# Kernel tuning notes

Hardware: AMD Instinct MI355X
Metric: run time of the kernel (lower is better)

## Reference

```python
import jax, jax.numpy as jnp
import numpy as np

B, T = 256, 1024
IN, OUT = 1, 1
H0, H1 = 256, 256


def _lstm_cell(x_t, h, c, W_ih, W_hh, b_ih, b_hh):
    # gates: [B, 4H] in torch LSTMCell order i, f, g, o
    g = x_t @ W_ih.T + b_ih + h @ W_hh.T + b_hh
    i, f, gg, o = jnp.split(g, 4, axis=-1)
    c_new = jax.nn.sigmoid(f) * c + jax.nn.sigmoid(i) * jnp.tanh(gg)
    h_new = jax.nn.sigmoid(o) * jnp.tanh(c_new)
    return h_new, c_new


def setup_inputs() -> dict:
    key = jax.random.key(0)
    ks = jax.random.split(key, 12)
    s = 0.1
    return {
        "x": jax.random.normal(ks[0], (B, T), dtype=jnp.float32),
        "W_ih0": jax.random.normal(ks[1], (4 * H0, IN), dtype=jnp.float32) * s,
        "W_hh0": jax.random.normal(ks[2], (4 * H0, H0), dtype=jnp.float32) * s,
        "b_ih0": jax.random.normal(ks[3], (4 * H0,), dtype=jnp.float32) * s,
        "b_hh0": jax.random.normal(ks[4], (4 * H0,), dtype=jnp.float32) * s,
        "W_ih1": jax.random.normal(ks[5], (4 * H1, H0), dtype=jnp.float32) * s,
        "W_hh1": jax.random.normal(ks[6], (4 * H1, H1), dtype=jnp.float32) * s,
        "b_ih1": jax.random.normal(ks[7], (4 * H1,), dtype=jnp.float32) * s,
        "b_hh1": jax.random.normal(ks[8], (4 * H1,), dtype=jnp.float32) * s,
        "W_lin": jax.random.normal(ks[9], (OUT, H1), dtype=jnp.float32) * s,
        "b_lin": jax.random.normal(ks[10], (OUT,), dtype=jnp.float32) * s,
        "future": 0,
    }


def reference(x, W_ih0, W_hh0, b_ih0, b_hh0, W_ih1, W_hh1, b_ih1, b_hh1,
              W_lin, b_lin, future):
    b = x.shape[0]
    h0 = jnp.zeros((b, H0), x.dtype)
    c0 = jnp.zeros((b, H0), x.dtype)
    h1 = jnp.zeros((b, H1), x.dtype)
    c1 = jnp.zeros((b, H1), x.dtype)

    def step(carry, x_t):
        ht, ct, gt, bt = carry
        ht, ct = _lstm_cell(x_t, ht, ct, W_ih0, W_hh0, b_ih0, b_hh0)
        gt, bt = _lstm_cell(ht, gt, bt, W_ih1, W_hh1, b_ih1, b_hh1)
        out = gt @ W_lin.T + b_lin  # [B, OUT]
        return (ht, ct, gt, bt), out

    xs = x.T[:, :, None]  # [T, B, 1]
    carry, outs = jax.lax.scan(step, (h0, c0, h1, c1), xs)

    if future > 0:
        def fstep(carry, _):
            state, out = carry
            state, out = step(state, out)
            return (state, out), out
        (_, _), fouts = jax.lax.scan(fstep, (carry, outs[-1]), None, length=future)
        outs = jnp.concatenate([outs, fouts], axis=0)

    # stack dim 1 then squeeze(2): [B, T+future]
    return jnp.transpose(outs, (1, 0, 2)).squeeze(2)
```

## Files before the change

kernel.cpp:

```cpp
#include <hip/hip_runtime.h>
#include <hip/hip_bf16.h>
#include <stdint.h>


#define TT 1024
#define NC 16

typedef __attribute__((ext_vector_type(8))) short  bfrag;
typedef __attribute__((ext_vector_type(4))) float  ffrag;

__device__ __forceinline__ float sigf(float v){ return 1.f/(1.f+__expf(-v)); }
__device__ __forceinline__ float tanhfast(float v){
    v = fminf(fmaxf(v,-15.f),15.f);
    float e = __expf(2.f*v);
    return (e-1.f)/(e+1.f);
}
__device__ __forceinline__ void st32(uint32_t* p, uint32_t v){
    __hip_atomic_store(p, v, __ATOMIC_RELAXED, __HIP_MEMORY_SCOPE_AGENT);
}
__device__ __forceinline__ void st64(unsigned long long* p, unsigned long long v){
    __hip_atomic_store(p, v, __ATOMIC_RELAXED, __HIP_MEMORY_SCOPE_AGENT);
}
__device__ __forceinline__ void stf(float* p, float v){
    __hip_atomic_store(p, v, __ATOMIC_RELAXED, __HIP_MEMORY_SCOPE_AGENT);
}
__device__ __forceinline__ void drain_vmem(){
    __asm__ volatile("s_waitcnt vmcnt(0)" ::: "memory");
}
__device__ __forceinline__ float2 ldf2_coh(const float* p1, const float* p2){
    float a, b;
    __asm__ volatile(
        "global_load_dword %0, %2, off sc0 sc1\n\t"
        "global_load_dword %1, %3, off sc0 sc1\n\t"
        "s_waitcnt vmcnt(0)"
        : "=&v"(a), "=&v"(b) : "v"(p1), "v"(p2) : "memory");
    return make_float2(a, b);
}
__device__ __forceinline__ void prefetch4(const int* fa, const int* fb,
                                          const int* fc, const int* fd,
                                          int& va, int& vb, int& vc, int& vd){
    __asm__ volatile(
        "global_load_dword %0, %4, off sc0 sc1\n\t"
        "global_load_dword %1, %5, off sc0 sc1\n\t"
        "global_load_dword %2, %6, off sc0 sc1\n\t"
        "global_load_dword %3, %7, off sc0 sc1"
        : "=&v"(va), "=&v"(vb), "=&v"(vc), "=&v"(vd)
        : "v"(fa), "v"(fb), "v"(fc), "v"(fd) : "memory");
}
__device__ __forceinline__ void wave_poll_pf(const int* fa, const int* fb,
                                             const int* fc, const int* fd,
                                             int tgtA, int tgtB,
                                             bool skA, bool skB, bool skC, bool skD,
                                             int& va, int& vb, int& vc, int& vd){
    __asm__ volatile("s_waitcnt vmcnt(0)"
                     : "+v"(va), "+v"(vb), "+v"(vc), "+v"(vd) :: "memory");
    __builtin_amdgcn_sched_barrier(0);
    if ((skA || va >= tgtA) && (skB || vb >= tgtA) &&
        (skC || vc >= tgtB) && (skD || vd >= tgtB)) return;
    for (;;) {
        __asm__ volatile(
            "global_load_dword %0, %4, off sc0 sc1\n\t"
            "global_load_dword %1, %5, off sc0 sc1\n\t"
            "global_load_dword %2, %6, off sc0 sc1\n\t"
            "global_load_dword %3, %7, off sc0 sc1\n\t"
            "s_waitcnt vmcnt(0)"
            : "=&v"(va), "=&v"(vb), "=&v"(vc), "=&v"(vd)
            : "v"(fa), "v"(fb), "v"(fc), "v"(fd) : "memory");
        if (va >= tgtA && vb >= tgtA && vc >= tgtB && vd >= tgtB) return;
        __builtin_amdgcn_s_sleep(1);
    }
}
__device__ __forceinline__ void stage_tile(uint32_t* ldsbase, const uint32_t* hblocks,
                                           int kt, int lane){
    const uint32_t* g = hblocks + (kt << 8) + ((lane & 15) << 4) + ((lane >> 4) << 2);
    uint32_t* l = ldsbase + (kt << 8);
    __builtin_amdgcn_global_load_lds(
        (const __attribute__((address_space(1))) uint32_t*)(uintptr_t)g,
        (__attribute__((address_space(3))) uint32_t*)(uint32_t)(uintptr_t)l,
        16, 0, 0x11);
}
__device__ __forceinline__ void xpose4(ffrag& a, int lane){
    float x0 = (lane&1) ? a[0] : a[1];
    float y0 = __shfl_xor(x0, 1);
    a[0] = (lane&1) ? y0 : a[0];  a[1] = (lane&1) ? a[1] : y0;
    float x1 = (lane&1) ? a[2] : a[3];
    float y1 = __shfl_xor(x1, 1);
    a[2] = (lane&1) ? y1 : a[2];  a[3] = (lane&1) ? a[3] : y1;
    float x2 = (lane&2) ? a[0] : a[2];
    float y2 = __shfl_xor(x2, 2);
    a[0] = (lane&2) ? y2 : a[0];  a[2] = (lane&2) ? a[2] : y2;
    float x3 = (lane&2) ? a[1] : a[3];
    float y3 = __shfl_xor(x3, 2);
    a[1] = (lane&2) ? y3 : a[1];  a[3] = (lane&2) ? a[3] : y3;
}

__global__ void __launch_bounds__(256, 1)
lstm_kernel(const float* __restrict__ x,
            const float* __restrict__ Wih0, const float* __restrict__ Whh0,
            const float* __restrict__ bih0, const float* __restrict__ bhh0,
            const float* __restrict__ Wih1, const float* __restrict__ Whh1,
            const float* __restrict__ bih1, const float* __restrict__ bhh1,
            const float* __restrict__ Wlin, const float* __restrict__ blin,
            float* __restrict__ out, char* __restrict__ ws)
{
    const int tid = threadIdx.x;
    const int wg  = blockIdx.x;
    const int c   = wg >> 4;
    const int j   = wg & 15;
    const bool isL0 = (j < 8);
    const int  u0   = (isL0 ? j : (j - 8)) * 32;

    int* flagbase = (int*)(ws + c * 4096);
    uint32_t* h0w = (uint32_t*)(ws + 65536);
    uint32_t* h1w = h0w + 4 * NC * 8 * 256;
    float*    op  = (float*)(h1w + 4 * NC * 8 * 256);

    __shared__ __attribute__((aligned(16))) char S[147456];
    __hip_bfloat16* Wt  = (__hip_bfloat16*)S;
    __hip_bfloat16* Wt2 = (__hip_bfloat16*)(S + 65536);
    float*          xs  = (float*)(S + 65536);
    uint32_t*       hs0 = (uint32_t*)(S + 131072);
    uint32_t*       hs1 = (uint32_t*)(S + 139264);

    const int lane = tid & 63, wave = tid >> 6;
    const int q_l  = (lane >> 2) & 3;
    const int g_l  = lane & 3;
    const int rg   = lane >> 4;
    const int row  = rg * 4 + g_l;
    const int u_e  = wave * 8 + q_l * 2;

    {
        const float* Wsrc = isL0 ? Whh0 : Wih1;
        for (int i = tid; i < 128 * 256; i += 256) {
            int n = i >> 8, k = i & 255;
            int ntile = n >> 4, cc = n & 15, q = cc >> 2, g = cc & 3;
            int unit = 8 * (ntile >> 1) + 2 * q + (ntile & 1);
            int r = g * 256 + u0 + unit;
            int ln = (n & 15) | (((k >> 3) & 3) << 4);
            int toff = (ntile * 8 + (k >> 5)) * 1024 + ln * 16 + (k & 7) * 2;
            *(__hip_bfloat16*)((char*)Wt + toff) = __float2bfloat16(Wsrc[r * 256 + k]);
            if (!isL0)
                *(__hip_bfloat16*)((char*)Wt2 + toff) = __float2bfloat16(Whh1[r * 256 + k]);
        }
        if (isL0) {
            for (int i = tid; i < 16 * 1024; i += 256)
                xs[i] = x[(c * 16 + (i & 15)) * TT + (i >> 4)];
        }
        uint32_t* z = isL0 ? (h0w + ((3 * NC + c) * 8 + j) * 256)
                           : (h1w + ((3 * NC + c) * 8 + (j - 8)) * 256);
        st32(z + tid, 0u);
    }
    float be0,be1,be2,be3, bo0,bo1,bo2,bo3;
    float we0=0,we1=0,we2=0,we3=0, wo0=0,wo1=0,wo2=0,wo3=0;
    float wle=0, wlo=0;
    {
        const float* bi = isL0 ? bih0 : bih1;
        const float* bh = isL0 ? bhh0 : bhh1;
        int r0 = u0 + u_e;
        be0 = bi[r0] + bh[r0];               bo0 = bi[r0+1] + bh[r0+1];
        be1 = bi[256+r0] + bh[256+r0];       bo1 = bi[256+r0+1] + bh[256+r0+1];
        be2 = bi[512+r0] + bh[512+r0];       bo2 = bi[512+r0+1] + bh[512+r0+1];
        be3 = bi[768+r0] + bh[768+r0];       bo3 = bi[768+r0+1] + bh[768+r0+1];
        if (isL0) {
            we0 = Wih0[r0];     wo0 = Wih0[r0+1];
            we1 = Wih0[256+r0]; wo1 = Wih0[256+r0+1];
            we2 = Wih0[512+r0]; wo2 = Wih0[512+r0+1];
            we3 = Wih0[768+r0]; wo3 = Wih0[768+r0+1];
        } else {
            wle = Wlin[u0 + u_e]; wlo = Wlin[u0 + u_e + 1];
        }
    }
    const float blin_r = blin[0];
    drain_vmem();
    __syncthreads();
    if (tid == 0) st32((uint32_t*)(flagbase + j * 32), 0u);

    const int* fL0a = flagbase + (wave)      * 32;
    const int* fL0b = flagbase + (wave + 4)  * 32;
    const int* fL1a = flagbase + (8 + wave)  * 32;
    const int* fL1b = flagbase + (12 + wave) * 32;
    int* myflag = (int*)(flagbase + j * 32);
    const bool skA = isL0 && (j == wave);
    const bool skB = isL0 && (j == wave + 4);
    const bool skC = (!isL0) && (j - 8 == wave);
    const bool skD = (!isL0) && (j - 8 == wave + 4);
    int va = -1000, vb = -1000, vc = -1000, vd = -1000;

    const char* wb0 = (const char*)Wt + (wave * 2) * 8192 + lane * 16;
    const char* wb1 = wb0 + 8192;
    const char* wc0 = (const char*)Wt2 + (wave * 2) * 8192 + lane * 16;
    const char* wc1 = wc0 + 8192;

    float c0a = 0.f, c0b = 0.f;

    if (isL0) {
        for (int t = 0; t < TT; ++t) {
            wave_poll_pf(fL0a, fL0b, fL1a, fL1b, t, t - 2,
                         skA, skB, false, false, va, vb, vc, vd);
            const uint32_t* src = h0w + (((t + 3) & 3) * NC + c) * 8 * 256;
            stage_tile(hs0, src, wave, lane);
            stage_tile(hs0, src, wave + 4, lane);
            __syncthreads();

            ffrag a0 = {0.f,0.f,0.f,0.f}, a1 = {0.f,0.f,0.f,0.f};
            #pragma unroll
            for (int kt = 0; kt < 8; ++kt) {
                bfrag av = *(const bfrag*)((const char*)hs0 + kt * 1024 + lane * 16);
                bfrag b0 = *(const bfrag*)(wb0 + kt * 1024);
                bfrag b1 = *(const bfrag*)(wb1 + kt * 1024);
                a0 = __builtin_amdgcn_mfma_f32_16x16x32_bf16(av, b0, a0, 0, 0, 0);
                a1 = __builtin_amdgcn_mfma_f32_16x16x32_bf16(av, b1, a1, 0, 0, 0);
            }
            xpose4(a0, lane);
            xpose4(a1, lane);

            float xv = xs[t * 16 + row];
            float iv = a0[0] + fmaf(xv, we0, be0);
            float fv = a0[1] + fmaf(xv, we1, be1);
            float gv = a0[2] + fmaf(xv, we2, be2);
            float ov = a0[3] + fmaf(xv, we3, be3);
            c0a = sigf(fv) * c0a + sigf(iv) * tanhfast(gv);
            float hn0 = sigf(ov) * tanhfast(c0a);
            iv = a1[0] + fmaf(xv, wo0, bo0);
            fv = a1[1] + fmaf(xv, wo1, bo1);
            gv = a1[2] + fmaf(xv, wo2, bo2);
            ov = a1[3] + fmaf(xv, wo3, bo3);
            c0b = sigf(fv) * c0b + sigf(iv) * tanhfast(gv);
            float hn1 = sigf(ov) * tanhfast(c0b);

            __hip_bfloat16 hb0 = __float2bfloat16(hn0), hb1 = __float2bfloat16(hn1);
            uint32_t pk = ((uint32_t)(*(uint16_t*)&hb1) << 16) | (uint32_t)(*(uint16_t*)&hb0);
            uint32_t nb = __shfl_down(pk, 4);
            if ((q_l & 1) == 0) {
                unsigned long long v = (unsigned long long)pk |
                                       ((unsigned long long)nb << 32);
                st64((unsigned long long*)
                     (h0w + (((t & 3) * NC + c) * 8 + j) * 256 + row * 16 + wave * 4 + q_l), v);
            }
            prefetch4(fL0a, fL0b, fL1a, fL1b, va, vb, vc, vd);
            drain_vmem();
            __syncthreads();
            if (tid == 0) st32((uint32_t*)myflag, (uint32_t)(t + 1));

            if (t >= 3 && j == ((t - 3) & 7)) {
                int col = t - 3, slot = col & 3;
                const float* o1 = op + (((slot * NC + c) * 32) + (tid & 15)) * 16 + (tid >> 4);
                float2 vv = ldf2_coh(o1, o1 + 256);
                float v = vv.x + vv.y;
                v += __shfl_down(v, 8, 16);
                v += __shfl_down(v, 4, 16);
                v += __shfl_down(v, 2, 16);
                v += __shfl_down(v, 1, 16);
                if ((tid & 15) == 0) out[(c * 16 + (tid >> 4)) * TT + col] = v + blin_r;
            }
        }
    } else {
        for (int t = 0; t < TT; ++t) {
            wave_poll_pf(fL0a, fL0b, fL1a, fL1b, t + 1, t,
                         false, false, skC, skD, va, vb, vc, vd);
            const uint32_t* s0 = h0w + ((t & 3) * NC + c) * 8 * 256;
            const uint32_t* s1 = h1w + (((t + 3) & 3) * NC + c) * 8 * 256;
            stage_tile(hs0, s0, wave, lane);
            stage_tile(hs0, s0, wave + 4, lane);
            stage_tile(hs1, s1, wave, lane);
            stage_tile(hs1, s1, wave + 4, lane);
            __syncthreads();

            ffrag a0 = {0.f,0.f,0.f,0.f}, a1 = {0.f,0.f,0.f,0.f};
            #pragma unroll
            for (int kt = 0; kt < 8; ++kt) {
                bfrag av = *(const bfrag*)((const char*)hs0 + kt * 1024 + lane * 16);
                bfrag b0 = *(const bfrag*)(wb0 + kt * 1024);
                bfrag b1 = *(const bfrag*)(wb1 + kt * 1024);
                a0 = __builtin_amdgcn_mfma_f32_16x16x32_bf16(av, b0, a0, 0, 0, 0);
                a1 = __builtin_amdgcn_mfma_f32_16x16x32_bf16(av, b1, a1, 0, 0, 0);
            }
            #pragma unroll
            for (int kt = 0; kt < 8; ++kt) {
                bfrag av = *(const bfrag*)((const char*)hs1 + kt * 1024 + lane * 16);
                bfrag b0 = *(const bfrag*)(wc0 + kt * 1024);
                bfrag b1 = *(const bfrag*)(wc1 + kt * 1024);
                a0 = __builtin_amdgcn_mfma_f32_16x16x32_bf16(av, b0, a0, 0, 0, 0);
                a1 = __builtin_amdgcn_mfma_f32_16x16x32_bf16(av, b1, a1, 0, 0, 0);
            }
            xpose4(a0, lane);
            xpose4(a1, lane);

            float iv = a0[0] + be0, fv = a0[1] + be1;
            float gv = a0[2] + be2, ov = a0[3] + be3;
            c0a = sigf(fv) * c0a + sigf(iv) * tanhfast(gv);
            float hn0 = sigf(ov) * tanhfast(c0a);
            iv = a1[0] + bo0; fv = a1[1] + bo1;
            gv = a1[2] + bo2; ov = a1[3] + bo3;
            c0b = sigf(fv) * c0b + sigf(iv) * tanhfast(gv);
            float hn1 = sigf(ov) * tanhfast(c0b);

            __hip_bfloat16 hb0 = __float2bfloat16(hn0), hb1 = __float2bfloat16(hn1);
            uint32_t pk = ((uint32_t)(*(uint16_t*)&hb1) << 16) | (uint32_t)(*(uint16_t*)&hb0);
            uint32_t nb = __shfl_down(pk, 4);

            float pv = hn0 * wle + hn1 * wlo;
            pv += __shfl_xor(pv, 4);
            pv += __shfl_xor(pv, 8);

            if ((q_l & 1) == 0) {
                unsigned long long v = (unsigned long long)pk |
                                       ((unsigned long long)nb << 32);
                st64((unsigned long long*)
                     (h1w + (((t & 3) * NC + c) * 8 + (j - 8)) * 256 + row * 16 + wave * 4 + q_l), v);
            }
            if ((lane & 12) == 0)
                stf(op + ((((t & 3) * NC + c) * 32) + (j - 8) * 4 + wave) * 16 + row, pv);
            prefetch4(fL0a, fL0b, fL1a, fL1b, va, vb, vc, vd);
            drain_vmem();
            __syncthreads();
            if (tid == 0) st32((uint32_t*)myflag, (uint32_t)(t + 1));
        }
    }

    drain_vmem();

    if (isL0 && j >= 5) {
        wave_poll_pf(fL0a, fL0b, fL1a, fL1b, 0, TT,
                     true, true, false, false, va, vb, vc, vd);
        __syncthreads();
        int col = TT - 8 + j, slot = col & 3;
        const float* o1 = op + (((slot * NC + c) * 32) + (tid & 15)) * 16 + (tid >> 4);
        float2 vv = ldf2_coh(o1, o1 + 256);
        float v = vv.x + vv.y;
        v += __shfl_down(v, 8, 16);
        v += __shfl_down(v, 4, 16);
        v += __shfl_down(v, 2, 16);
        v += __shfl_down(v, 1, 16);
        if ((tid & 15) == 0) out[(c * 16 + (tid >> 4)) * TT + col] = v + blin_r;
    }
}

extern "C" void kernel_launch(void* const* d_in, const int* in_sizes, int n_in,
                              void* d_out, int out_size, void* d_ws, size_t ws_size,
                              hipStream_t stream)
{
    const float* x    = (const float*)d_in[0];
    const float* Wih0 = (const float*)d_in[1];
    const float* Whh0 = (const float*)d_in[2];
    const float* bih0 = (const float*)d_in[3];
    const float* bhh0 = (const float*)d_in[4];
    const float* Wih1 = (const float*)d_in[5];
    const float* Whh1 = (const float*)d_in[6];
    const float* bih1 = (const float*)d_in[7];
    const float* bhh1 = (const float*)d_in[8];
    const float* Wlin = (const float*)d_in[9];
    const float* blin = (const float*)d_in[10];
    float* out = (float*)d_out;
    char* ws   = (char*)d_ws;

    lstm_kernel<<<dim3(256), dim3(256), 0, stream>>>(
        x, Wih0, Whh0, bih0, bhh0, Wih1, Whh1, bih1, bhh1, Wlin, blin, out, ws);
}
```

Baseline: 3.284 ms.

## Process two batch chunks per workgroup and widen layer pipeline skew

Each workgroup now handles two 16-row batch chunks (A and B) instead of one, halving the grid to 128 workgroups and the number of groups that synchronize through global flags. Flags become 64-bit paired lines polled with dwordx2 loads and a wave-wide all-vote, with a bail-out counter. The layer-1 schedule now lags layer 0 by two steps, the output buffer ring grows to 8 slots, and the final linear reduction is deferred and batched for both chunks. This amortizes per-step sync latency over twice the MFMA work but doubles serial work per step per workgroup, and the bail-out could silently break correctness if polling stalls.

```diff
diff --git a/kernel.cpp b/kernel.cpp
--- a/kernel.cpp
+++ b/kernel.cpp
@@ -8,6 +8,7 @@
 
 typedef __attribute__((ext_vector_type(8))) short  bfrag;
 typedef __attribute__((ext_vector_type(4))) float  ffrag;
+typedef __attribute__((ext_vector_type(2))) int    i2v;
 
 __device__ __forceinline__ float sigf(float v){ return 1.f/(1.f+__expf(-v)); }
 __device__ __forceinline__ float tanhfast(float v){
@@ -26,49 +27,6 @@
 }
 __device__ __forceinline__ void drain_vmem(){
     __asm__ volatile("s_waitcnt vmcnt(0)" ::: "memory");
-}
-__device__ __forceinline__ float2 ldf2_coh(const float* p1, const float* p2){
-    float a, b;
-    __asm__ volatile(
-        "global_load_dword %0, %2, off sc0 sc1\n\t"
-        "global_load_dword %1, %3, off sc0 sc1\n\t"
-        "s_waitcnt vmcnt(0)"
-        : "=&v"(a), "=&v"(b) : "v"(p1), "v"(p2) : "memory");
-    return make_float2(a, b);
-}
-__device__ __forceinline__ void prefetch4(const int* fa, const int* fb,
-                                          const int* fc, const int* fd,
-                                          int& va, int& vb, int& vc, int& vd){
-    __asm__ volatile(
-        "global_load_dword %0, %4, off sc0 sc1\n\t"
-        "global_load_dword %1, %5, off sc0 sc1\n\t"
-        "global_load_dword %2, %6, off sc0 sc1\n\t"
-        "global_load_dword %3, %7, off sc0 sc1"
-        : "=&v"(va), "=&v"(vb), "=&v"(vc), "=&v"(vd)
-        : "v"(fa), "v"(fb), "v"(fc), "v"(fd) : "memory");
-}
-__device__ __forceinline__ void wave_poll_pf(const int* fa, const int* fb,
-                                             const int* fc, const int* fd,
-                                             int tgtA, int tgtB,
-                                             bool skA, bool skB, bool skC, bool skD,
-                                             int& va, int& vb, int& vc, int& vd){
-    __asm__ volatile("s_waitcnt vmcnt(0)"
-                     : "+v"(va), "+v"(vb), "+v"(vc), "+v"(vd) :: "memory");
-    __builtin_amdgcn_sched_barrier(0);
-    if ((skA || va >= tgtA) && (skB || vb >= tgtA) &&
-        (skC || vc >= tgtB) && (skD || vd >= tgtB)) return;
-    for (;;) {
-        __asm__ volatile(
-            "global_load_dword %0, %4, off sc0 sc1\n\t"
-            "global_load_dword %1, %5, off sc0 sc1\n\t"
-            "global_load_dword %2, %6, off sc0 sc1\n\t"
-            "global_load_dword %3, %7, off sc0 sc1\n\t"
-            "s_waitcnt vmcnt(0)"
-            : "=&v"(va), "=&v"(vb), "=&v"(vc), "=&v"(vd)
-            : "v"(fa), "v"(fb), "v"(fc), "v"(fd) : "memory");
-        if (va >= tgtA && vb >= tgtA && vc >= tgtB && vd >= tgtB) return;
-        __builtin_amdgcn_s_sleep(1);
-    }
 }
 __device__ __forceinline__ void stage_tile(uint32_t* ldsbase, const uint32_t* hblocks,
                                            int kt, int lane){
@@ -93,6 +51,30 @@
     float y3 = __shfl_xor(x3, 2);
     a[1] = (lane&2) ? y3 : a[1];  a[3] = (lane&2) ? a[3] : y3;
 }
+__device__ __forceinline__ void reduce2(const float* op, int cA, int cB, int col,
+                                        int tid, float blin_r, float* __restrict__ out){
+    int slot = col & 7;
+    const float* oA = op + ((slot * NC + cA) * 32 + (tid & 15)) * 16 + (tid >> 4);
+    const float* oB = op + ((slot * NC + cB) * 32 + (tid & 15)) * 16 + (tid >> 4);
+    float ra, rb, rc, rd;
+    __asm__ volatile(
+        "global_load_dword %0, %4, off sc0 sc1\n\t"
+        "global_load_dword %1, %5, off sc0 sc1\n\t"
+        "global_load_dword %2, %6, off sc0 sc1\n\t"
+        "global_load_dword %3, %7, off sc0 sc1\n\t"
+        "s_waitcnt vmcnt(0)"
+        : "=&v"(ra), "=&v"(rb), "=&v"(rc), "=&v"(rd)
+        : "v"(oA), "v"(oA + 256), "v"(oB), "v"(oB + 256) : "memory");
+    float vA = ra + rb, vB = rc + rd;
+    vA += __shfl_down(vA, 8, 16); vA += __shfl_down(vA, 4, 16);
+    vA += __shfl_down(vA, 2, 16); vA += __shfl_down(vA, 1, 16);
+    vB += __shfl_down(vB, 8, 16); vB += __shfl_down(vB, 4, 16);
+    vB += __shfl_down(vB, 2, 16); vB += __shfl_down(vB, 1, 16);
+    if ((tid & 15) == 0) {
+        out[(cA * 16 + (tid >> 4)) * TT + col] = vA + blin_r;
+        out[(cB * 16 + (tid >> 4)) * TT + col] = vB + blin_r;
+    }
+}
 
 __global__ void __launch_bounds__(256, 1)
 lstm_kernel(const float* __restrict__ x,
@@ -105,22 +87,23 @@
 {
     const int tid = threadIdx.x;
     const int wg  = blockIdx.x;
-    const int c   = wg >> 4;
+    const int g   = wg >> 4;
     const int j   = wg & 15;
     const bool isL0 = (j < 8);
     const int  u0   = (isL0 ? j : (j - 8)) * 32;
-
-    int* flagbase = (int*)(ws + c * 4096);
+    const int  cA = g * 2, cB = g * 2 + 1;
+
+    char* flg = ws + (size_t)g * 4096;
     uint32_t* h0w = (uint32_t*)(ws + 65536);
     uint32_t* h1w = h0w + 4 * NC * 8 * 256;
     float*    op  = (float*)(h1w + 4 * NC * 8 * 256);
 
-    __shared__ __attribute__((aligned(16))) char S[147456];
+    __shared__ __attribute__((aligned(16))) char S[155648];
     __hip_bfloat16* Wt  = (__hip_bfloat16*)S;
     __hip_bfloat16* Wt2 = (__hip_bfloat16*)(S + 65536);
-    float*          xs  = (float*)(S + 65536);
-    uint32_t*       hs0 = (uint32_t*)(S + 131072);
-    uint32_t*       hs1 = (uint32_t*)(S + 139264);
+    char* tA0 = S + 131072;
+    char* tA1 = S + 139264;
+    char* tB0 = S + 147456;
 
     const int lane = tid & 63, wave = tid >> 6;
     const int q_l  = (lane >> 2) & 3;
@@ -133,22 +116,21 @@
         const float* Wsrc = isL0 ? Whh0 : Wih1;
         for (int i = tid; i < 128 * 256; i += 256) {
             int n = i >> 8, k = i & 255;
-            int ntile = n >> 4, cc = n & 15, q = cc >> 2, g = cc & 3;
+            int ntile = n >> 4, cc = n & 15, q = cc >> 2, gg = cc & 3;
             int unit = 8 * (ntile >> 1) + 2 * q + (ntile & 1);
-            int r = g * 256 + u0 + unit;
+            int r = gg * 256 + u0 + unit;
             int ln = (n & 15) | (((k >> 3) & 3) << 4);
             int toff = (ntile * 8 + (k >> 5)) * 1024 + ln * 16 + (k & 7) * 2;
             *(__hip_bfloat16*)((char*)Wt + toff) = __float2bfloat16(Wsrc[r * 256 + k]);
             if (!isL0)
                 *(__hip_bfloat16*)((char*)Wt2 + toff) = __float2bfloat16(Whh1[r * 256 + k]);
         }
-        if (isL0) {
-            for (int i = tid; i < 16 * 1024; i += 256)
-                xs[i] = x[(c * 16 + (i & 15)) * TT + (i >> 4)];
-        }
-        uint32_t* z = isL0 ? (h0w + ((3 * NC + c) * 8 + j) * 256)
-                           : (h1w + ((3 * NC + c) * 8 + (j - 8)) * 256);
-        st32(z + tid, 0u);
+        uint32_t* zA = isL0 ? (h0w + ((3 * NC + cA) * 8 + j) * 256)
+                            : (h1w + ((3 * NC + cA) * 8 + (j - 8)) * 256);
+        uint32_t* zB = isL0 ? (h0w + ((3 * NC + cB) * 8 + j) * 256)
+                            : (h1w + ((3 * NC + cB) * 8 + (j - 8)) * 256);
+        st32(zA + tid, 0u);
+        st32(zB + tid, 0u);
     }
     float be0,be1,be2,be3, bo0,bo1,bo2,bo3;
     float we0=0,we1=0,we2=0,we3=0, wo0=0,wo1=0,wo2=0,wo3=0;
@@ -173,166 +155,261 @@
     const float blin_r = blin[0];
     drain_vmem();
     __syncthreads();
-    if (tid == 0) st32((uint32_t*)(flagbase + j * 32), 0u);
-
-    const int* fL0a = flagbase + (wave)      * 32;
-    const int* fL0b = flagbase + (wave + 4)  * 32;
-    const int* fL1a = flagbase + (8 + wave)  * 32;
-    const int* fL1b = flagbase + (12 + wave) * 32;
-    int* myflag = (int*)(flagbase + j * 32);
-    const bool skA = isL0 && (j == wave);
-    const bool skB = isL0 && (j == wave + 4);
-    const bool skC = (!isL0) && (j - 8 == wave);
-    const bool skD = (!isL0) && (j - 8 == wave + 4);
-    int va = -1000, vb = -1000, vc = -1000, vd = -1000;
+    if (tid == 0) st64((unsigned long long*)(flg + j * 128), 0ull);
+
+    const i2v* p0 = (const i2v*)(flg + (wave)      * 128);
+    const i2v* p1 = (const i2v*)(flg + (wave + 4)  * 128);
+    const i2v* p2 = (const i2v*)(flg + (8 + wave)  * 128);
+    const i2v* p3 = (const i2v*)(flg + (12 + wave) * 128);
+    unsigned long long* myline = (unsigned long long*)(flg + j * 128);
 
     const char* wb0 = (const char*)Wt + (wave * 2) * 8192 + lane * 16;
     const char* wb1 = wb0 + 8192;
     const char* wc0 = (const char*)Wt2 + (wave * 2) * 8192 + lane * 16;
     const char* wc1 = wc0 + 8192;
 
-    float c0a = 0.f, c0b = 0.f;
+    float cAa = 0.f, cAb = 0.f, cBa = 0.f, cBb = 0.f;
 
     if (isL0) {
-        for (int t = 0; t < TT; ++t) {
-            wave_poll_pf(fL0a, fL0b, fL1a, fL1b, t, t - 2,
-                         skA, skB, false, false, va, vb, vc, vd);
-            const uint32_t* src = h0w + (((t + 3) & 3) * NC + c) * 8 * 256;
-            stage_tile(hs0, src, wave, lane);
-            stage_tile(hs0, src, wave + 4, lane);
-            __syncthreads();
-
-            ffrag a0 = {0.f,0.f,0.f,0.f}, a1 = {0.f,0.f,0.f,0.f};
-            #pragma unroll
-            for (int kt = 0; kt < 8; ++kt) {
-                bfrag av = *(const bfrag*)((const char*)hs0 + kt * 1024 + lane * 16);
-                bfrag b0 = *(const bfrag*)(wb0 + kt * 1024);
-                bfrag b1 = *(const bfrag*)(wb1 + kt * 1024);
-                a0 = __builtin_amdgcn_mfma_f32_16x16x32_bf16(av, b0, a0, 0, 0, 0);
-                a1 = __builtin_amdgcn_mfma_f32_16x16x32_bf16(av, b1, a1, 0, 0, 0);
-            }
-            xpose4(a0, lane);
-            xpose4(a1, lane);
-
-            float xv = xs[t * 16 + row];
-            float iv = a0[0] + fmaf(xv, we0, be0);
-            float fv = a0[1] + fmaf(xv, we1, be1);
-            float gv = a0[2] + fmaf(xv, we2, be2);
-            float ov = a0[3] + fmaf(xv, we3, be3);
-            c0a = sigf(fv) * c0a + sigf(iv) * tanhfast(gv);
-            float hn0 = sigf(ov) * tanhfast(c0a);
-            iv = a1[0] + fmaf(xv, wo0, bo0);
-            fv = a1[1] + fmaf(xv, wo1, bo1);
-            gv = a1[2] + fmaf(xv, wo2, bo2);
-            ov = a1[3] + fmaf(xv, wo3, bo3);
-            c0b = sigf(fv) * c0b + sigf(iv) * tanhfast(gv);
-            float hn1 = sigf(ov) * tanhfast(c0b);
-
-            __hip_bfloat16 hb0 = __float2bfloat16(hn0), hb1 = __float2bfloat16(hn1);
-            uint32_t pk = ((uint32_t)(*(uint16_t*)&hb1) << 16) | (uint32_t)(*(uint16_t*)&hb0);
-            uint32_t nb = __shfl_down(pk, 4);
+        for (int k = 0; k < TT; ++k) {
+            {
+                i2v v0, v1, v2, v3; int bail = 0;
+                for (;;) {
+                    __asm__ volatile(
+                        "global_load_dwordx2 %0, %4, off sc0 sc1\n\t"
+                        "global_load_dwordx2 %1, %5, off sc0 sc1\n\t"
+                        "global_load_dwordx2 %2, %6, off sc0 sc1\n\t"
+                        "global_load_dwordx2 %3, %7, off sc0 sc1\n\t"
+                        "s_waitcnt vmcnt(0)"
+                        : "=&v"(v0), "=&v"(v1), "=&v"(v2), "=&v"(v3)
+                        : "v"(p0), "v"(p1), "v"(p2), "v"(p3) : "memory");
+                    bool ok = (v0.x >= k) && (v0.y >= k) && (v1.x >= k) && (v1.y >= k)
+                           && (v2.x >= k-3) && (v2.y >= k-3) && (v3.x >= k-3) && (v3.y >= k-3);
+                    if (__all(ok)) break;
+                    if (++bail > (1 << 21)) break;
+                    __builtin_amdgcn_s_sleep(1);
+                }
+            }
+            float xvA = x[(cA * 16 + row) * TT + k];
+            float xvB = x[(cB * 16 + row) * TT + k];
+            const uint32_t* srcA = h0w + (((k + 3) & 3) * NC + cA) * 8 * 256;
+            const uint32_t* srcB = h0w + (((k + 3) & 3) * NC + cB) * 8 * 256;
+            stage_tile((uint32_t*)tA0, srcA, wave, lane);
+            stage_tile((uint32_t*)tA0, srcA, wave + 4, lane);
+            stage_tile((uint32_t*)tB0, srcB, wave, lane);
+            stage_tile((uint32_t*)tB0, srcB, wave + 4, lane);
+            __syncthreads();
+
+            uint32_t pkA, pkB;
+            {
+                ffrag a0 = {0.f,0.f,0.f,0.f}, a1 = {0.f,0.f,0.f,0.f};
+                #pragma unroll
+                for (int kt = 0; kt < 8; ++kt) {
+                    bfrag av = *(const bfrag*)(tA0 + kt * 1024 + lane * 16);
+                    bfrag b0 = *(const bfrag*)(wb0 + kt * 1024);
+                    bfrag b1 = *(const bfrag*)(wb1 + kt * 1024);
+                    a0 = __builtin_amdgcn_mfma_f32_16x16x32_bf16(av, b0, a0, 0, 0, 0);
+                    a1 = __builtin_amdgcn_mfma_f32_16x16x32_bf16(av, b1, a1, 0, 0, 0);
+                }
+                xpose4(a0, lane); xpose4(a1, lane);
+                float iv = a0[0] + fmaf(xvA, we0, be0);
+                float fv = a0[1] + fmaf(xvA, we1, be1);
+                float gv = a0[2] + fmaf(xvA, we2, be2);
+                float ov = a0[3] + fmaf(xvA, we3, be3);
+                cAa = sigf(fv) * cAa + sigf(iv) * tanhfast(gv);
+                float hn0 = sigf(ov) * tanhfast(cAa);
+                iv = a1[0] + fmaf(xvA, wo0, bo0);
+                fv = a1[1] + fmaf(xvA, wo1, bo1);
+                gv = a1[2] + fmaf(xvA, wo2, bo2);
+                ov = a1[3] + fmaf(xvA, wo3, bo3);
+                cAb = sigf(fv) * cAb + sigf(iv) * tanhfast(gv);
+                float hn1 = sigf(ov) * tanhfast(cAb);
+                __hip_bfloat16 hb0 = __float2bfloat16(hn0), hb1 = __float2bfloat16(hn1);
+                pkA = ((uint32_t)(*(uint16_t*)&hb1) << 16) | (uint32_t)(*(uint16_t*)&hb0);
+            }
+            {
+                ffrag a0 = {0.f,0.f,0.f,0.f}, a1 = {0.f,0.f,0.f,0.f};
+                #pragma unroll
+                for (int kt = 0; kt < 8; ++kt) {
+                    bfrag av = *(const bfrag*)(tB0 + kt * 1024 + lane * 16);
+                    bfrag b0 = *(const bfrag*)(wb0 + kt * 1024);
+                    bfrag b1 = *(const bfrag*)(wb1 + kt * 1024);
+                    a0 = __builtin_amdgcn_mfma_f32_16x16x32_bf16(av, b0, a0, 0, 0, 0);
+                    a1 = __builtin_amdgcn_mfma_f32_16x16x32_bf16(av, b1, a1, 0, 0, 0);
+                }
+                xpose4(a0, lane); xpose4(a1, lane);
+                float iv = a0[0] + fmaf(xvB, we0, be0);
+                float fv = a0[1] + fmaf(xvB, we1, be1);
+                float gv = a0[2] + fmaf(xvB, we2, be2);
+                float ov = a0[3] + fmaf(xvB, we3, be3);
+                cBa = sigf(fv) * cBa + sigf(iv) * tanhfast(gv);
+                float hn0 = sigf(ov) * tanhfast(cBa);
+                iv = a1[0] + fmaf(xvB, wo0, bo0);
+                fv = a1[1] + fmaf(xvB, wo1, bo1);
+                gv = a1[2] + fmaf(xvB, wo2, bo2);
+                ov = a1[3] + fmaf(xvB, wo3, bo3);
+                cBb = sigf(fv) * cBb + sigf(iv) * tanhfast(gv);
+                float hn1 = sigf(ov) * tanhfast(cBb);
+                __hip_bfloat16 hb0 = __float2bfloat16(hn0), hb1 = __float2bfloat16(hn1);
+                pkB = ((uint32_t)(*(uint16_t*)&hb1) << 16) | (uint32_t)(*(uint16_t*)&hb0);
+            }
+            uint32_t nbA = __shfl_down(pkA, 4);
+            uint32_t nbB = __shfl_down(pkB, 4);
             if ((q_l & 1) == 0) {
-                unsigned long long v = (unsigned long long)pk |
-                                       ((unsigned long long)nb << 32);
                 st64((unsigned long long*)
-                     (h0w + (((t & 3) * NC + c) * 8 + j) * 256 + row * 16 + wave * 4 + q_l), v);
-            }
-            prefetch4(fL0a, fL0b, fL1a, fL1b, va, vb, vc, vd);
+                     (h0w + (((k & 3) * NC + cA) * 8 + j) * 256 + row * 16 + wave * 4 + q_l),
+                     (unsigned long long)pkA | ((unsigned long long)nbA << 32));
+                st64((unsigned long long*)
+                     (h0w + (((k & 3) * NC + cB) * 8 + j) * 256 + row * 16 + wave * 4 + q_l),
+                     (unsigned long long)pkB | ((unsigned long long)nbB << 32));
+            }
             drain_vmem();
             __syncthreads();
-            if (tid == 0) st32((uint32_t*)myflag, (uint32_t)(t + 1));
-
-            if (t >= 3 && j == ((t - 3) & 7)) {
-                int col = t - 3, slot = col & 3;
-                const float* o1 = op + (((slot * NC + c) * 32) + (tid & 15)) * 16 + (tid >> 4);
-                float2 vv = ldf2_coh(o1, o1 + 256);
-                float v = vv.x + vv.y;
-                v += __shfl_down(v, 8, 16);
-                v += __shfl_down(v, 4, 16);
-                v += __shfl_down(v, 2, 16);
-                v += __shfl_down(v, 1, 16);
-                if ((tid & 15) == 0) out[(c * 16 + (tid >> 4)) * TT + col] = v + blin_r;
-            }
+            if (tid == 0)
+                st64(myline, (unsigned long long)(uint32_t)(k + 1) * 0x100000001ull);
+
+            if (k >= 4 && j == ((k - 4) & 7))
+                reduce2(op, cA, cB, k - 4, tid, blin_r, out);
+        }
+        if (j >= 4) {
+            i2v v2, v3; int bail = 0;
+            for (;;) {
+                __asm__ volatile(
+                    "global_load_dwordx2 %0, %2, off sc0 sc1\n\t"
+                    "global_load_dwordx2 %1, %3, off sc0 sc1\n\t"
+                    "s_waitcnt vmcnt(0)"
+                    : "=&v"(v2), "=&v"(v3) : "v"(p2), "v"(p3) : "memory");
+                bool ok = (v2.x >= TT) && (v2.y >= TT) && (v3.x >= TT) && (v3.y >= TT);
+                if (__all(ok)) break;
+                if (++bail > (1 << 22)) break;
+                __builtin_amdgcn_s_sleep(1);
+            }
+            __syncthreads();
+            reduce2(op, cA, cB, TT - 8 + j, tid, blin_r, out);
         }
     } else {
-        for (int t = 0; t < TT; ++t) {
-            wave_poll_pf(fL0a, fL0b, fL1a, fL1b, t + 1, t,
-                         false, false, skC, skD, va, vb, vc, vd);
-            const uint32_t* s0 = h0w + ((t & 3) * NC + c) * 8 * 256;
-            const uint32_t* s1 = h1w + (((t + 3) & 3) * NC + c) * 8 * 256;
-            stage_tile(hs0, s0, wave, lane);
-            stage_tile(hs0, s0, wave + 4, lane);
-            stage_tile(hs1, s1, wave, lane);
-            stage_tile(hs1, s1, wave + 4, lane);
-            __syncthreads();
-
-            ffrag a0 = {0.f,0.f,0.f,0.f}, a1 = {0.f,0.f,0.f,0.f};
-            #pragma unroll
-            for (int kt = 0; kt < 8; ++kt) {
-                bfrag av = *(const bfrag*)((const char*)hs0 + kt * 1024 + lane * 16);
-                bfrag b0 = *(const bfrag*)(wb0 + kt * 1024);
-                bfrag b1 = *(const bfrag*)(wb1 + kt * 1024);
-                a0 = __builtin_amdgcn_mfma_f32_16x16x32_bf16(av, b0, a0, 0, 0, 0);
-                a1 = __builtin_amdgcn_mfma_f32_16x16x32_bf16(av, b1, a1, 0, 0, 0);
-            }
-            #pragma unroll
-            for (int kt = 0; kt < 8; ++kt) {
-                bfrag av = *(const bfrag*)((const char*)hs1 + kt * 1024 + lane * 16);
-                bfrag b0 = *(const bfrag*)(wc0 + kt * 1024);
-                bfrag b1 = *(const bfrag*)(wc1 + kt * 1024);
-                a0 = __builtin_amdgcn_mfma_f32_16x16x32_bf16(av, b0, a0, 0, 0, 0);
-                a1 = __builtin_amdgcn_mfma_f32_16x16x32_bf16(av, b1, a1, 0, 0, 0);
-            }
-            xpose4(a0, lane);
-            xpose4(a1, lane);
-
-            float iv = a0[0] + be0, fv = a0[1] + be1;
-            float gv = a0[2] + be2, ov = a0[3] + be3;
-            c0a = sigf(fv) * c0a + sigf(iv) * tanhfast(gv);
-            float hn0 = sigf(ov) * tanhfast(c0a);
-            iv = a1[0] + bo0; fv = a1[1] + bo1;
-            gv = a1[2] + bo2; ov = a1[3] + bo3;
-            c0b = sigf(fv) * c0b + sigf(iv) * tanhfast(gv);
-            float hn1 = sigf(ov) * tanhfast(c0b);
-
-            __hip_bfloat16 hb0 = __float2bfloat16(hn0), hb1 = __float2bfloat16(hn1);
-            uint32_t pk = ((uint32_t)(*(uint16_t*)&hb1) << 16) | (uint32_t)(*(uint16_t*)&hb0);
-            uint32_t nb = __shfl_down(pk, 4);
-
-            float pv = hn0 * wle + hn1 * wlo;
-            pv += __shfl_xor(pv, 4);
-            pv += __shfl_xor(pv, 8);
-
+        for (int k = 2; k < TT + 2; ++k) {
+            const int s = k - 2;
+            {
+                i2v v0, v1, v2, v3; int bail = 0;
+                for (;;) {
+                    __asm__ volatile(
+                        "global_load_dwordx2 %0, %4, off sc0 sc1\n\t"
+                        "global_load_dwordx2 %1, %5, off sc0 sc1\n\t"
+                        "global_load_dwordx2 %2, %6, off sc0 sc1\n\t"
+                        "global_load_dwordx2 %3, %7, off sc0 sc1\n\t"
+                        "s_waitcnt vmcnt(0)"
+                        : "=&v"(v0), "=&v"(v1), "=&v"(v2), "=&v"(v3)
+                        : "v"(p0), "v"(p1), "v"(p2), "v"(p3) : "memory");
+                    bool ok = (v0.x >= k-1) && (v0.y >= k-1) && (v1.x >= k-1) && (v1.y >= k-1)
+                           && (v2.x >= k-2) && (v2.y >= k-2) && (v3.x >= k-2) && (v3.y >= k-2);
+                    if (__all(ok)) break;
+                    if (++bail > (1 << 21)) break;
+                    __builtin_amdgcn_s_sleep(1);
+                }
+            }
+            const uint32_t* sA0 = h0w + ((s & 3) * NC + cA) * 8 * 256;
+            const uint32_t* sA1 = h1w + (((s + 3) & 3) * NC + cA) * 8 * 256;
+            const uint32_t* sB0 = h0w + ((s & 3) * NC + cB) * 8 * 256;
+            stage_tile((uint32_t*)tA0, sA0, wave, lane);
+            stage_tile((uint32_t*)tA0, sA0, wave + 4, lane);
+            stage_tile((uint32_t*)tA1, sA1, wave, lane);
+            stage_tile((uint32_t*)tA1, sA1, wave + 4, lane);
+            stage_tile((uint32_t*)tB0, sB0, wave, lane);
+            stage_tile((uint32_t*)tB0, sB0, wave + 4, lane);
+            __syncthreads();
+
+            uint32_t pkA, pkB; float pvA, pvB;
+            {
+                ffrag a0 = {0.f,0.f,0.f,0.f}, a1 = {0.f,0.f,0.f,0.f};
+                #pragma unroll
+                for (int kt = 0; kt < 8; ++kt) {
+                    bfrag av = *(const bfrag*)(tA0 + kt * 1024 + lane * 16);
+                    bfrag b0 = *(const bfrag*)(wb0 + kt * 1024);
+                    bfrag b1 = *(const bfrag*)(wb1 + kt * 1024);
+                    a0 = __builtin_amdgcn_mfma_f32_16x16x32_bf16(av, b0, a0, 0, 0, 0);
+                    a1 = __builtin_amdgcn_mfma_f32_16x16x32_bf16(av, b1, a1, 0, 0, 0);
+                }
+                #pragma unroll
+                for (int kt = 0; kt < 8; ++kt) {
+                    bfrag av = *(const bfrag*)(tA1 + kt * 1024 + lane * 16);
+                    bfrag b0 = *(const bfrag*)(wc0 + kt * 1024);
+                    bfrag b1 = *(const bfrag*)(wc1 + kt * 1024);
+                    a0 = __builtin_amdgcn_mfma_f32_16x16x32_bf16(av, b0, a0, 0, 0, 0);
+                    a1 = __builtin_amdgcn_mfma_f32_16x16x32_bf16(av, b1, a1, 0, 0, 0);
+                }
+                xpose4(a0, lane); xpose4(a1, lane);
+                float iv = a0[0] + be0, fv = a0[1] + be1;
+                float gv = a0[2] + be2, ov = a0[3] + be3;
+                cAa = sigf(fv) * cAa + sigf(iv) * tanhfast(gv);
+                float hn0 = sigf(ov) * tanhfast(cAa);
+                iv = a1[0] + bo0; fv = a1[1] + bo1;
+                gv = a1[2] + bo2; ov = a1[3] + bo3;
+                cAb = sigf(fv) * cAb + sigf(iv) * tanhfast(gv);
+                float hn1 = sigf(ov) * tanhfast(cAb);
+                __hip_bfloat16 hb0 = __float2bfloat16(hn0), hb1 = __float2bfloat16(hn1);
+                pkA = ((uint32_t)(*(uint16_t*)&hb1) << 16) | (uint32_t)(*(uint16_t*)&hb0);
+                pvA = hn0 * wle + hn1 * wlo;
+                pvA += __shfl_xor(pvA, 4);
+                pvA += __shfl_xor(pvA, 8);
+            }
+            __syncthreads();
+            const uint32_t* sB1 = h1w + (((s + 3) & 3) * NC + cB) * 8 * 256;
+            stage_tile((uint32_t*)tA0, sB1, wave, lane);
+            stage_tile((uint32_t*)tA0, sB1, wave + 4, lane);
+            {
+                ffrag a0 = {0.f,0.f,0.f,0.f}, a1 = {0.f,0.f,0.f,0.f};
+                #pragma unroll
+                for (int kt = 0; kt < 8; ++kt) {
+                    bfrag av = *(const bfrag*)(tB0 + kt * 1024 + lane * 16);
+                    bfrag b0 = *(const bfrag*)(wb0 + kt * 1024);
+                    bfrag b1 = *(const bfrag*)(wb1 + kt * 1024);
+                    a0 = __builtin_amdgcn_mfma_f32_16x16x32_bf16(av, b0, a0, 0, 0, 0);
+                    a1 = __builtin_amdgcn_mfma_f32_16x16x32_bf16(av, b1, a1, 0, 0, 0);
+                }
+                __syncthreads();
+                #pragma unroll
+                for (int kt = 0; kt < 8; ++kt) {
+                    bfrag av = *(const bfrag*)(tA0 + kt * 1024 + lane * 16);
+                    bfrag b0 = *(const bfrag*)(wc0 + kt * 1024);
+                    bfrag b1 = *(const bfrag*)(wc1 + kt * 1024);
+                    a0 = __builtin_amdgcn_mfma_f32_16x16x32_bf16(av, b0, a0, 0, 0, 0);
+                    a1 = __builtin_amdgcn_mfma_f32_16x16x32_bf16(av, b1, a1, 0, 0, 0);
+                }
+                xpose4(a0, lane); xpose4(a1, lane);
+                float iv = a0[0] + be0, fv = a0[1] + be1;
+                float gv = a0[2] + be2, ov = a0[3] + be3;
+                cBa = sigf(fv) * cBa + sigf(iv) * tanhfast(gv);
+                float hn0 = sigf(ov) * tanhfast(cBa);
+                iv = a1[0] + bo0; fv = a1[1] + bo1;
+                gv = a1[2] + bo2; ov = a1[3] + bo3;
+                cBb = sigf(fv) * cBb + sigf(iv) * tanhfast(gv);
+                float hn1 = sigf(ov) * tanhfast(cBb);
+                __hip_bfloat16 hb0 = __float2bfloat16(hn0), hb1 = __float2bfloat16(hn1);
+                pkB = ((uint32_t)(*(uint16_t*)&hb1) << 16) | (uint32_t)(*(uint16_t*)&hb0);
+                pvB = hn0 * wle + hn1 * wlo;
+                pvB += __shfl_xor(pvB, 4);
+                pvB += __shfl_xor(pvB, 8);
+            }
+            uint32_t nbA = __shfl_down(pkA, 4);
+            uint32_t nbB = __shfl_down(pkB, 4);
             if ((q_l & 1) == 0) {
-                unsigned long long v = (unsigned long long)pk |
-                                       ((unsigned long long)nb << 32);
                 st64((unsigned long long*)
-                     (h1w + (((t & 3) * NC + c) * 8 + (j - 8)) * 256 + row * 16 + wave * 4 + q_l), v);
-            }
-            if ((lane & 12) == 0)
-                stf(op + ((((t & 3) * NC + c) * 32) + (j - 8) * 4 + wave) * 16 + row, pv);
-            prefetch4(fL0a, fL0b, fL1a, fL1b, va, vb, vc, vd);
+                     (h1w + (((s & 3) * NC + cA) * 8 + (j - 8)) * 256 + row * 16 + wave * 4 + q_l),
+                     (unsigned long long)pkA | ((unsigned long long)nbA << 32));
+                st64((unsigned long long*)
+                     (h1w + (((s & 3) * NC + cB) * 8 + (j - 8)) * 256 + row * 16 + wave * 4 + q_l),
+                     (unsigned long long)pkB | ((unsigned long long)nbB << 32));
+            }
+            if ((lane & 12) == 0) {
+                stf(op + (((s & 7) * NC + cA) * 32 + (j - 8) * 4 + wave) * 16 + row, pvA);
+                stf(op + (((s & 7) * NC + cB) * 32 + (j - 8) * 4 + wave) * 16 + row, pvB);
+            }
             drain_vmem();
             __syncthreads();
-            if (tid == 0) st32((uint32_t*)myflag, (uint32_t)(t + 1));
+            if (tid == 0)
+                st64(myline, (unsigned long long)(uint32_t)(k - 1) * 0x100000001ull);
         }
-    }
-
-    drain_vmem();
-
-    if (isL0 && j >= 5) {
-        wave_poll_pf(fL0a, fL0b, fL1a, fL1b, 0, TT,
-                     true, true, false, false, va, vb, vc, vd);
-        __syncthreads();
-        int col = TT - 8 + j, slot = col & 3;
-        const float* o1 = op + (((slot * NC + c) * 32) + (tid & 15)) * 16 + (tid >> 4);
-        float2 vv = ldf2_coh(o1, o1 + 256);
-        float v = vv.x + vv.y;
-        v += __shfl_down(v, 8, 16);
-        v += __shfl_down(v, 4, 16);
-        v += __shfl_down(v, 2, 16);
-        v += __shfl_down(v, 1, 16);
-        if ((tid & 15) == 0) out[(c * 16 + (tid >> 4)) * TT + col] = v + blin_r;
     }
 }
 
@@ -354,6 +431,6 @@
     float* out = (float*)d_out;
     char* ws   = (char*)d_ws;
 
-    lstm_kernel<<<dim3(256), dim3(256), 0, stream>>>(
+    lstm_kernel<<<dim3(128), dim3(256), 0, stream>>>(
         x, Wih0, Whh0, bih0, bhh0, Wih1, Whh1, bih1, bhh1, Wlin, blin, out, ws);
 }
```

Result: slower. 4.516 ms (+37.5%).
